# Kernel tuning notes

Measured on AMD Instinct MI355X. Metric: run time of the kernel, lower is better.

The kernel has to match this reference:

```python
import jax, jax.numpy as jnp
import numpy as np

N1, C, T1, V = 16, 64, 512, 25
NH, DK, DV, BD = 8, 64, 64, 64
DKH, DVH = DK // NH, DV // NH
NB = T1 // BD


def rel_to_abs(x):
    # x: (..., L, 2L-1) -> (..., L, L)  (rel-shift trick)
    *lead, L, _ = x.shape
    x = jnp.pad(x, [(0, 0)] * (x.ndim - 1) + [(0, 1)])      # (..., L, 2L)
    x = x.reshape(*lead, L * 2 * L)
    x = jnp.pad(x, [(0, 0)] * (x.ndim - 1) + [(0, L - 1)])
    x = x.reshape(*lead, L + 1, 2 * L - 1)
    return x[..., :L, L - 1:]


def setup_inputs() -> dict:
    key = jax.random.key(0)
    ks = jax.random.split(key, 6)
    return {
        "x": jax.random.normal(ks[0], (N1, C, T1, V), jnp.float32),
        "w_qkv": jax.random.normal(ks[1], (2 * DK + DV, C), jnp.float32) * 0.05,
        "b_qkv": jax.random.normal(ks[2], (2 * DK + DV,), jnp.float32) * 0.01,
        "w_out": jax.random.normal(ks[3], (DV, DV), jnp.float32) * 0.05,
        "b_out": jax.random.normal(ks[4], (DV,), jnp.float32) * 0.01,
        "key_rel": jax.random.normal(ks[5], (2 * BD - 1, DKH), jnp.float32),
    }


def reference(x, w_qkv, b_qkv, w_out, b_out, key_rel):
    B = N1 * V
    # (N1,C,T1,V) -> (N1*V, C, T1); 1x1 qkv conv == GEMM over channels
    xr = x.transpose(0, 3, 1, 2).reshape(B, C, T1)
    qkv = jnp.einsum('oc,bct->bot', w_qkv, xr) + b_qkv[None, :, None]
    q, k, v = qkv[:, :DK], qkv[:, DK:2 * DK], qkv[:, 2 * DK:]
    # split heads and blocks: (B, NH, dh, NB, BD); all blocks vectorized
    q = q.reshape(B, NH, DKH, NB, BD) * (DKH ** -0.5)
    k = k.reshape(B, NH, DKH, NB, BD)
    v = v.reshape(B, NH, DVH, NB, BD)
    logits = jnp.einsum('bhdnt,bhdns->bhnts', q, k)          # (B,NH,NB,BD,BD)
    # relative position logits (rel-shift)
    qb = q.transpose(0, 1, 3, 4, 2)                          # (B,NH,NB,BD,DKH)
    rel = jnp.einsum('bhntd,md->bhntm', qb, key_rel)         # (B,NH,NB,BD,2BD-1)
    logits = logits + rel_to_abs(rel)
    weights = jax.nn.softmax(logits, axis=-1)
    out = jnp.einsum('bhnts,bhdns->bhdnt', weights, v)       # (B,NH,DVH,NB,BD)
    # combine heads (head-major channels) and blocks along T
    out = out.reshape(B, DV, T1)
    ao = jnp.einsum('oc,bct->bot', w_out, out) + b_out[None, :, None]
    ao = ao.reshape(N1, V, DV, T1).transpose(0, 2, 3, 1)     # (N1,DV,T1,V)
    return jax.nn.relu(ao + x)
```

## Files before the change

### kernel.cpp

```cpp
#include <hip/hip_runtime.h>
#include <math.h>

#define Vc 25
#define QSCALE 0.5100697243f

typedef short bf16x8 __attribute__((ext_vector_type(8), may_alias));
typedef unsigned int u32x2a __attribute__((ext_vector_type(2), may_alias));
typedef float f32x4 __attribute__((ext_vector_type(4)));

#define FENCE() asm volatile("" ::: "memory")

__device__ __forceinline__ unsigned short f2bf(float f) {
    unsigned u = __builtin_bit_cast(unsigned, f);
    u = (u + 0x7fff + ((u >> 16) & 1)) >> 16;
    return (unsigned short)u;
}
__device__ __forceinline__ unsigned short f2bf_fast(float f) {
    unsigned u = __builtin_bit_cast(unsigned, f) + 0x8000u;
    return (unsigned short)(u >> 16);
}
__device__ __forceinline__ unsigned pkbf(float lo, float hi) {
    unsigned a = __builtin_bit_cast(unsigned, lo) + 0x8000u;
    unsigned b = __builtin_bit_cast(unsigned, hi) + 0x8000u;
    return __builtin_amdgcn_perm(b, a, 0x07060302);
}
__device__ __forceinline__ float bf2f(unsigned short h) {
    unsigned u = ((unsigned)h) << 16;
    return __builtin_bit_cast(float, u);
}

template<int CTRL>
__device__ __forceinline__ float dpp_add(float x) {
    int xi = __builtin_bit_cast(int, x);
    int yi = __builtin_amdgcn_update_dpp(0, xi, CTRL, 0xf, 0xf, true);
    return x + __builtin_bit_cast(float, yi);
}
__device__ __forceinline__ float row_sum16(float s) {
    s = dpp_add<0xB1>(s);
    s = dpp_add<0x4E>(s);
    s = dpp_add<0x141>(s);
    s = dpp_add<0x140>(s);
    return s;
}

#define WQA_O 0
#define BQ_O  12288
#define KRT_O 12672
#define WOA_O 13760

__global__ void prep_kernel(const float* __restrict__ w_qkv, const float* __restrict__ b_qkv,
                            const float* __restrict__ w_out, const float* __restrict__ key_rel,
                            unsigned short* __restrict__ ws)
{
    const int gid = blockIdx.x * 256 + threadIdx.x;
    const int gsz = gridDim.x * 256;
    for (int id = gid; id < 12288; id += gsz) {
        int j = id & 7, lane = (id >> 3) & 63, ks = (id >> 9) & 1, mt = id >> 10;
        int m = mt * 16 + (lane & 15);
        int k = ks * 32 + (lane >> 4) * 8 + j;
        ws[WQA_O + id] = f2bf(w_qkv[m * 64 + k] * (m < 64 ? QSCALE : 1.f));
    }
    float* bq = (float*)(ws + BQ_O);
    for (int id = gid; id < 192; id += gsz)
        bq[id] = b_qkv[id] * (id < 64 ? QSCALE : 1.f);
    for (int id = gid; id < 1088; id += gsz) {
        int d = id & 7, m = id >> 3;
        ws[KRT_O + id] = (m < 127) ? f2bf(key_rel[m * 8 + d]) : (unsigned short)0;
    }
    for (int id = gid; id < 4096; id += gsz) {
        int j = id & 7, lane = (id >> 3) & 63, mtg = id >> 9;
        int m = (mtg & 3) * 16 + (lane & 15);
        int k = (mtg >> 2) * 32 + (lane >> 4) * 8 + j;
        ws[WOA_O + id] = f2bf(w_out[m * 64 + k]);
    }
}

#define QT_O   0
#define KT_O   4096
#define VS_O   8192
#define OT_O   12800
#define SCR_O  15360
#define SMEM_U16 19968

__global__ __launch_bounds__(256, 4)
void tcn_attn(const float* __restrict__ x, const float* __restrict__ b_out,
              const unsigned short* __restrict__ ws, float* __restrict__ y)
{
    __shared__ unsigned short sm[SMEM_U16];

    const int tid  = threadIdx.x;
    const int lane = tid & 63;
    const int w    = tid >> 6;
    const int li   = lane & 15;
    const int lq   = lane >> 4;
    const int koff = lq * 8;
    const int n    = blockIdx.x;
    const int b    = blockIdx.y;
    const int n1   = b / Vc;
    const int v    = b - n1 * Vc;
    const int t0   = n * 64;
    const int trow = 16 * w + li;
    const unsigned scr = SCR_O + w * 1152;

    const bf16x8 z8 = {0,0,0,0,0,0,0,0};
    const f32x4  z4 = {0.f,0.f,0.f,0.f};

    for (int i = tid; i < 1920; i += 256)
        *(bf16x8*)(sm + i * 8) = z8;

    float xres[16];
    f32x4 pacc[4];
    #pragma unroll
    for (int mt = 0; mt < 4; ++mt)
        #pragma unroll
        for (int r = 0; r < 4; ++r) {
            int o = mt * 16 + lq * 4 + r;
            xres[mt * 4 + r] = x[((n1 * 64 + o) * 512 + t0 + 16 * w + li) * Vc + v];
            pacc[mt][r] = b_out[o];
        }

    #pragma unroll
    for (int mt = 0; mt < 4; ++mt)
        #pragma unroll
        for (int r = 0; r < 4; ++r)
            sm[SCR_O + (16 * w + li) * 72 + mt * 16 + 4 * lq + r] = f2bf_fast(xres[mt * 4 + r]);
    __syncthreads();

    const unsigned short* wq = ws + WQA_O;
    const float* bq = (const float*)(ws + BQ_O);
    #pragma unroll
    for (int sec = 0; sec < 3; ++sec) {
        const int mt = sec * 4 + w;
        bf16x8 a0 = *(const bf16x8*)(wq + ((mt * 2 + 0) * 64 + lane) * 8);
        bf16x8 a1 = *(const bf16x8*)(wq + ((mt * 2 + 1) * 64 + lane) * 8);
        f32x4 acc[4];
        #pragma unroll
        for (int nt = 0; nt < 4; ++nt) {
            #pragma unroll
            for (int r = 0; r < 4; ++r) acc[nt][r] = bq[mt * 16 + lq * 4 + r];
            bf16x8 b0 = *(const bf16x8*)(sm + SCR_O + (16 * nt + li) * 72 + koff);
            bf16x8 b1 = *(const bf16x8*)(sm + SCR_O + (16 * nt + li) * 72 + 32 + koff);
            acc[nt] = __builtin_amdgcn_mfma_f32_16x16x32_bf16(a0, b0, acc[nt], 0, 0, 0);
            acc[nt] = __builtin_amdgcn_mfma_f32_16x16x32_bf16(a1, b1, acc[nt], 0, 0, 0);
        }
        const int h2 = 2 * w + (lq >> 1);
        if (sec < 2) {
            const unsigned base = (sec == 0 ? QT_O : KT_O) + h2 * 512 + (lq & 1) * 4;
            #pragma unroll
            for (int nt = 0; nt < 4; ++nt) {
                u32x2a p;
                p.x = pkbf(acc[nt][0], acc[nt][1]);
                p.y = pkbf(acc[nt][2], acc[nt][3]);
                *(u32x2a*)(sm + base + (16 * nt + li) * 8) = p;
            }
        } else {
            #pragma unroll
            for (int nt = 0; nt < 4; ++nt)
                #pragma unroll
                for (int r = 0; r < 4; ++r)
                    sm[VS_O + h2 * 576 + ((lq & 1) * 4 + r) * 72 + 16 * nt + li] = f2bf_fast(acc[nt][r]);
        }
    }
    __syncthreads();

    bf16x8 br[5];
    #pragma unroll
    for (int j = 0; j < 5; ++j)
        br[j] = *(const bf16x8*)(ws + KRT_O + (16 * (3 - w + j) + li) * 8 + koff);

    int bidx[4];
    bool ghi[4];
    #pragma unroll
    for (int r = 0; r < 4; ++r) {
        int d = li - 4 * lq - r + 15;
        bidx[r] = ((lane & 48) | (d & 15)) << 2;
        ghi[r]  = d >= 16;
    }

    auto FRONT = [&](int h, f32x4* qk, f32x4* rl) {
        bf16x8 aq = *(const bf16x8*)(sm + QT_O + h * 512 + trow * 8 + koff);
        if (lane >= 16) aq = z8;
        #pragma unroll
        for (int nt = 0; nt < 4; ++nt) {
            bf16x8 bk = *(const bf16x8*)(sm + KT_O + h * 512 + (16 * nt + li) * 8 + koff);
            qk[nt] = __builtin_amdgcn_mfma_f32_16x16x32_bf16(aq, bk, z4, 0, 0, 0);
        }
        #pragma unroll
        for (int j = 0; j < 5; ++j)
            rl[j] = __builtin_amdgcn_mfma_f32_16x16x32_bf16(aq, br[j], z4, 0, 0, 0);
    };

    f32x4 qk[4], rl[5];
    FRONT(0, qk, rl);

    #pragma unroll
    for (int h = 0; h < 8; ++h) {
        f32x4 qkn[4], rln[5];
        if (h < 7) FRONT(h + 1, qkn, rln);
        bf16x8 ao[4];
        if ((h & 3) == 3) {
            const int g = h >> 2;
            #pragma unroll
            for (int mt = 0; mt < 4; ++mt)
                ao[mt] = *(const bf16x8*)(ws + WOA_O + ((g * 4 + mt) * 64 + lane) * 8);
        }
        float ex[4][4], lsum[4] = {0.f, 0.f, 0.f, 0.f};
        #pragma unroll
        for (int r = 0; r < 4; ++r) {
            float sr[5];
            #pragma unroll
            for (int j = 0; j < 5; ++j)
                sr[j] = __builtin_bit_cast(float,
                        __builtin_amdgcn_ds_bpermute(bidx[r], __builtin_bit_cast(int, rl[j][r])));
            #pragma unroll
            for (int nt = 0; nt < 4; ++nt) {
                float rv = ghi[r] ? sr[nt + 1] : sr[nt];
                float e = __builtin_amdgcn_exp2f(qk[nt][r] + rv);
                ex[nt][r] = e;
                lsum[r] += e;
            }
        }
        float linv[4];
        #pragma unroll
        for (int r = 0; r < 4; ++r)
            linv[r] = 1.0f / row_sum16(lsum[r]);
        #pragma unroll
        for (int nt = 0; nt < 4; ++nt)
            #pragma unroll
            for (int r = 0; r < 4; ++r)
                sm[scr + (4 * lq + r) * 72 + 16 * nt + li] = f2bf_fast(ex[nt][r]);
        FENCE();
        f32x4 av = z4;
        #pragma unroll
        for (int ks = 0; ks < 2; ++ks) {
            bf16x8 aa = *(const bf16x8*)(sm + scr + li * 72 + ks * 32 + koff);
            bf16x8 bv = *(const bf16x8*)(sm + VS_O + h * 576 + (li & 7) * 72 + ks * 32 + koff);
            av = __builtin_amdgcn_mfma_f32_16x16x32_bf16(aa, bv, av, 0, 0, 0);
        }
        if (li < 8) {
            #pragma unroll
            for (int r = 0; r < 4; ++r)
                sm[OT_O + (16 * w + 4 * lq + r) * 40 + (h & 3) * 8 + li] = f2bf_fast(av[r] * linv[r]);
        }
        if ((h & 3) == 3) {
            FENCE();
            bf16x8 bo = *(const bf16x8*)(sm + OT_O + trow * 40 + koff);
            #pragma unroll
            for (int mt = 0; mt < 4; ++mt)
                pacc[mt] = __builtin_amdgcn_mfma_f32_16x16x32_bf16(ao[mt], bo, pacc[mt], 0, 0, 0);
        }
        FENCE();
        if (h < 7) {
            #pragma unroll
            for (int i = 0; i < 4; ++i) qk[i] = qkn[i];
            #pragma unroll
            for (int j = 0; j < 5; ++j) rl[j] = rln[j];
        }
    }

    #pragma unroll
    for (int mt = 0; mt < 4; ++mt)
        #pragma unroll
        for (int r = 0; r < 4; ++r) {
            int o = mt * 16 + lq * 4 + r;
            int idx = ((n1 * 64 + o) * 512 + t0 + 16 * w + li) * Vc + v;
            y[idx] = fmaxf(pacc[mt][r] + xres[mt * 4 + r], 0.f);
        }
}

extern "C" void kernel_launch(void* const* d_in, const int* in_sizes, int n_in,
                              void* d_out, int out_size, void* d_ws, size_t ws_size,
                              hipStream_t stream) {
    const float* x       = (const float*)d_in[0];
    const float* w_qkv   = (const float*)d_in[1];
    const float* b_qkv   = (const float*)d_in[2];
    const float* w_out   = (const float*)d_in[3];
    const float* b_out   = (const float*)d_in[4];
    const float* key_rel = (const float*)d_in[5];
    float* y = (float*)d_out;
    unsigned short* ws = (unsigned short*)d_ws;

    prep_kernel<<<dim3(96), dim3(256), 0, stream>>>(w_qkv, b_qkv, w_out, key_rel, ws);
    dim3 grid(512 / 64, 400);
    tcn_attn<<<grid, dim3(256), 0, stream>>>(x, b_out, ws, y);
}
```

Measured before the change: 218.1 us.

## Split heads across two wave groups with 512-thread blocks

```diff
diff --git a/kernel.cpp b/kernel.cpp
--- a/kernel.cpp
+++ b/kernel.cpp
@@ -79,10 +79,10 @@
 #define KT_O   4096
 #define VS_O   8192
 #define OT_O   12800
-#define SCR_O  15360
-#define SMEM_U16 19968
-
-__global__ __launch_bounds__(256, 4)
+#define SCR_O  17408
+#define SMEM_U16 26624
+
+__global__ __launch_bounds__(512, 6)
 void tcn_attn(const float* __restrict__ x, const float* __restrict__ b_out,
               const unsigned short* __restrict__ ws, float* __restrict__ y)
 {
@@ -91,6 +91,8 @@
     const int tid  = threadIdx.x;
     const int lane = tid & 63;
     const int w    = tid >> 6;
+    const int rg   = w >> 1;
+    const int hg   = w & 1;
     const int li   = lane & 15;
     const int lq   = lane >> 4;
     const int koff = lq * 8;
@@ -99,66 +101,61 @@
     const int n1   = b / Vc;
     const int v    = b - n1 * Vc;
     const int t0   = n * 64;
-    const int trow = 16 * w + li;
+    const int trow = 16 * rg + li;
     const unsigned scr = SCR_O + w * 1152;
 
     const bf16x8 z8 = {0,0,0,0,0,0,0,0};
     const f32x4  z4 = {0.f,0.f,0.f,0.f};
 
-    for (int i = tid; i < 1920; i += 256)
+    for (int i = tid; i < 2176; i += 512)
         *(bf16x8*)(sm + i * 8) = z8;
 
-    float xres[16];
-    f32x4 pacc[4];
-    #pragma unroll
-    for (int mt = 0; mt < 4; ++mt)
+    float xres[8];
+    f32x4 pacc[2];
+    #pragma unroll
+    for (int mtl = 0; mtl < 2; ++mtl)
         #pragma unroll
         for (int r = 0; r < 4; ++r) {
-            int o = mt * 16 + lq * 4 + r;
-            xres[mt * 4 + r] = x[((n1 * 64 + o) * 512 + t0 + 16 * w + li) * Vc + v];
-            pacc[mt][r] = b_out[o];
-        }
-
-    #pragma unroll
-    for (int mt = 0; mt < 4; ++mt)
+            int o = hg * 32 + mtl * 16 + lq * 4 + r;
+            xres[mtl * 4 + r] = x[((n1 * 64 + o) * 512 + t0 + trow) * Vc + v];
+            pacc[mtl][r] = b_out[o];
+        }
+
+    #pragma unroll
+    for (int mtl = 0; mtl < 2; ++mtl)
         #pragma unroll
         for (int r = 0; r < 4; ++r)
-            sm[SCR_O + (16 * w + li) * 72 + mt * 16 + 4 * lq + r] = f2bf_fast(xres[mt * 4 + r]);
+            sm[SCR_O + trow * 72 + hg * 32 + mtl * 16 + 4 * lq + r] = f2bf_fast(xres[mtl * 4 + r]);
     __syncthreads();
 
     const unsigned short* wq = ws + WQA_O;
     const float* bq = (const float*)(ws + BQ_O);
     #pragma unroll
-    for (int sec = 0; sec < 3; ++sec) {
-        const int mt = sec * 4 + w;
+    for (int i = 0; i < 6; ++i) {
+        const int p  = 6 * w + i;
+        const int mt = p >> 2;
+        const int nt = p & 3;
         bf16x8 a0 = *(const bf16x8*)(wq + ((mt * 2 + 0) * 64 + lane) * 8);
         bf16x8 a1 = *(const bf16x8*)(wq + ((mt * 2 + 1) * 64 + lane) * 8);
-        f32x4 acc[4];
-        #pragma unroll
-        for (int nt = 0; nt < 4; ++nt) {
-            #pragma unroll
-            for (int r = 0; r < 4; ++r) acc[nt][r] = bq[mt * 16 + lq * 4 + r];
-            bf16x8 b0 = *(const bf16x8*)(sm + SCR_O + (16 * nt + li) * 72 + koff);
-            bf16x8 b1 = *(const bf16x8*)(sm + SCR_O + (16 * nt + li) * 72 + 32 + koff);
-            acc[nt] = __builtin_amdgcn_mfma_f32_16x16x32_bf16(a0, b0, acc[nt], 0, 0, 0);
-            acc[nt] = __builtin_amdgcn_mfma_f32_16x16x32_bf16(a1, b1, acc[nt], 0, 0, 0);
-        }
-        const int h2 = 2 * w + (lq >> 1);
-        if (sec < 2) {
-            const unsigned base = (sec == 0 ? QT_O : KT_O) + h2 * 512 + (lq & 1) * 4;
-            #pragma unroll
-            for (int nt = 0; nt < 4; ++nt) {
-                u32x2a p;
-                p.x = pkbf(acc[nt][0], acc[nt][1]);
-                p.y = pkbf(acc[nt][2], acc[nt][3]);
-                *(u32x2a*)(sm + base + (16 * nt + li) * 8) = p;
-            }
+        f32x4 acc;
+        #pragma unroll
+        for (int r = 0; r < 4; ++r) acc[r] = bq[mt * 16 + lq * 4 + r];
+        bf16x8 b0 = *(const bf16x8*)(sm + SCR_O + (16 * nt + li) * 72 + koff);
+        bf16x8 b1 = *(const bf16x8*)(sm + SCR_O + (16 * nt + li) * 72 + 32 + koff);
+        acc = __builtin_amdgcn_mfma_f32_16x16x32_bf16(a0, b0, acc, 0, 0, 0);
+        acc = __builtin_amdgcn_mfma_f32_16x16x32_bf16(a1, b1, acc, 0, 0, 0);
+        const int mt4 = mt & 3;
+        const int h2  = 2 * mt4 + (lq >> 1);
+        if (mt < 8) {
+            const unsigned base = (mt < 4 ? QT_O : KT_O) + h2 * 512 + (lq & 1) * 4;
+            u32x2a pk;
+            pk.x = pkbf(acc[0], acc[1]);
+            pk.y = pkbf(acc[2], acc[3]);
+            *(u32x2a*)(sm + base + (16 * nt + li) * 8) = pk;
         } else {
             #pragma unroll
-            for (int nt = 0; nt < 4; ++nt)
-                #pragma unroll
-                for (int r = 0; r < 4; ++r)
-                    sm[VS_O + h2 * 576 + ((lq & 1) * 4 + r) * 72 + 16 * nt + li] = f2bf_fast(acc[nt][r]);
+            for (int r = 0; r < 4; ++r)
+                sm[VS_O + h2 * 576 + ((lq & 1) * 4 + r) * 72 + 16 * nt + li] = f2bf_fast(acc[r]);
         }
     }
     __syncthreads();
@@ -166,7 +163,7 @@
     bf16x8 br[5];
     #pragma unroll
     for (int j = 0; j < 5; ++j)
-        br[j] = *(const bf16x8*)(ws + KRT_O + (16 * (3 - w + j) + li) * 8 + koff);
+        br[j] = *(const bf16x8*)(ws + KRT_O + (16 * (3 - rg + j) + li) * 8 + koff);
 
     int bidx[4];
     bool ghi[4];
@@ -191,19 +188,13 @@
     };
 
     f32x4 qk[4], rl[5];
-    FRONT(0, qk, rl);
-
-    #pragma unroll
-    for (int h = 0; h < 8; ++h) {
+    FRONT(hg * 4, qk, rl);
+
+    #pragma unroll
+    for (int hh = 0; hh < 4; ++hh) {
+        const int h = hg * 4 + hh;
         f32x4 qkn[4], rln[5];
-        if (h < 7) FRONT(h + 1, qkn, rln);
-        bf16x8 ao[4];
-        if ((h & 3) == 3) {
-            const int g = h >> 2;
-            #pragma unroll
-            for (int mt = 0; mt < 4; ++mt)
-                ao[mt] = *(const bf16x8*)(ws + WOA_O + ((g * 4 + mt) * 64 + lane) * 8);
-        }
+        if (hh < 3) FRONT(h + 1, qkn, rln);
         float ex[4][4], lsum[4] = {0.f, 0.f, 0.f, 0.f};
         #pragma unroll
         for (int r = 0; r < 4; ++r) {
@@ -240,17 +231,10 @@
         if (li < 8) {
             #pragma unroll
             for (int r = 0; r < 4; ++r)
-                sm[OT_O + (16 * w + 4 * lq + r) * 40 + (h & 3) * 8 + li] = f2bf_fast(av[r] * linv[r]);
-        }
-        if ((h & 3) == 3) {
-            FENCE();
-            bf16x8 bo = *(const bf16x8*)(sm + OT_O + trow * 40 + koff);
-            #pragma unroll
-            for (int mt = 0; mt < 4; ++mt)
-                pacc[mt] = __builtin_amdgcn_mfma_f32_16x16x32_bf16(ao[mt], bo, pacc[mt], 0, 0, 0);
+                sm[OT_O + (16 * rg + 4 * lq + r) * 72 + h * 8 + li] = f2bf_fast(av[r] * linv[r]);
         }
         FENCE();
-        if (h < 7) {
+        if (hh < 3) {
             #pragma unroll
             for (int i = 0; i < 4; ++i) qk[i] = qkn[i];
             #pragma unroll
@@ -258,13 +242,25 @@
         }
     }
 
-    #pragma unroll
-    for (int mt = 0; mt < 4; ++mt)
+    __syncthreads();
+    bf16x8 bo0 = *(const bf16x8*)(sm + OT_O + trow * 72 + koff);
+    bf16x8 bo1 = *(const bf16x8*)(sm + OT_O + trow * 72 + 32 + koff);
+    #pragma unroll
+    for (int mtl = 0; mtl < 2; ++mtl) {
+        const int gmt = hg * 2 + mtl;
+        bf16x8 a0 = *(const bf16x8*)(ws + WOA_O + ((0 + gmt) * 64 + lane) * 8);
+        bf16x8 a1 = *(const bf16x8*)(ws + WOA_O + ((4 + gmt) * 64 + lane) * 8);
+        pacc[mtl] = __builtin_amdgcn_mfma_f32_16x16x32_bf16(a0, bo0, pacc[mtl], 0, 0, 0);
+        pacc[mtl] = __builtin_amdgcn_mfma_f32_16x16x32_bf16(a1, bo1, pacc[mtl], 0, 0, 0);
+    }
+
+    #pragma unroll
+    for (int mtl = 0; mtl < 2; ++mtl)
         #pragma unroll
         for (int r = 0; r < 4; ++r) {
-            int o = mt * 16 + lq * 4 + r;
-            int idx = ((n1 * 64 + o) * 512 + t0 + 16 * w + li) * Vc + v;
-            y[idx] = fmaxf(pacc[mt][r] + xres[mt * 4 + r], 0.f);
+            int o = hg * 32 + mtl * 16 + lq * 4 + r;
+            int idx = ((n1 * 64 + o) * 512 + t0 + trow) * Vc + v;
+            y[idx] = fmaxf(pacc[mtl][r] + xres[mtl * 4 + r], 0.f);
         }
 }
 
@@ -282,5 +278,5 @@
 
     prep_kernel<<<dim3(96), dim3(256), 0, stream>>>(w_qkv, b_qkv, w_out, key_rel, ws);
     dim3 grid(512 / 64, 400);
-    tcn_attn<<<grid, dim3(256), 0, stream>>>(x, b_out, ws, y);
-}
+    tcn_attn<<<grid, dim3(512), 0, stream>>>(x, b_out, ws, y);
+}
```

Result: slower. 376.6 us (+72.6%).

## Convert attention kernel to persistent blocks pulling work items from an atomic queue

Applied to the files above, without the earlier changes.

```diff
diff --git a/kernel.cpp b/kernel.cpp
--- a/kernel.cpp
+++ b/kernel.cpp
@@ -3,6 +3,7 @@
 
 #define Vc 25
 #define QSCALE 0.5100697243f
+#define NITEMS 3200
 
 typedef short bf16x8 __attribute__((ext_vector_type(8), may_alias));
 typedef unsigned int u32x2a __attribute__((ext_vector_type(2), may_alias));
@@ -47,6 +48,7 @@
 #define BQ_O  12288
 #define KRT_O 12672
 #define WOA_O 13760
+#define CNT_O 17856
 
 __global__ void prep_kernel(const float* __restrict__ w_qkv, const float* __restrict__ b_qkv,
                             const float* __restrict__ w_out, const float* __restrict__ key_rel,
@@ -54,6 +56,7 @@
 {
     const int gid = blockIdx.x * 256 + threadIdx.x;
     const int gsz = gridDim.x * 256;
+    if (gid == 0) *(unsigned*)(ws + CNT_O) = 0u;
     for (int id = gid; id < 12288; id += gsz) {
         int j = id & 7, lane = (id >> 3) & 63, ks = (id >> 9) & 1, mt = id >> 10;
         int m = mt * 16 + (lane & 15);
@@ -84,9 +87,11 @@
 
 __global__ __launch_bounds__(256, 4)
 void tcn_attn(const float* __restrict__ x, const float* __restrict__ b_out,
-              const unsigned short* __restrict__ ws, float* __restrict__ y)
+              const unsigned short* __restrict__ ws, unsigned* __restrict__ cnt,
+              float* __restrict__ y)
 {
     __shared__ unsigned short sm[SMEM_U16];
+    __shared__ unsigned s_item;
 
     const int tid  = threadIdx.x;
     const int lane = tid & 63;
@@ -94,11 +99,6 @@
     const int li   = lane & 15;
     const int lq   = lane >> 4;
     const int koff = lq * 8;
-    const int n    = blockIdx.x;
-    const int b    = blockIdx.y;
-    const int n1   = b / Vc;
-    const int v    = b - n1 * Vc;
-    const int t0   = n * 64;
     const int trow = 16 * w + li;
     const unsigned scr = SCR_O + w * 1152;
 
@@ -108,60 +108,12 @@
     for (int i = tid; i < 1920; i += 256)
         *(bf16x8*)(sm + i * 8) = z8;
 
-    float xres[16];
-    f32x4 pacc[4];
+    float bias_r[16];
     #pragma unroll
     for (int mt = 0; mt < 4; ++mt)
         #pragma unroll
-        for (int r = 0; r < 4; ++r) {
-            int o = mt * 16 + lq * 4 + r;
-            xres[mt * 4 + r] = x[((n1 * 64 + o) * 512 + t0 + 16 * w + li) * Vc + v];
-            pacc[mt][r] = b_out[o];
-        }
-
-    #pragma unroll
-    for (int mt = 0; mt < 4; ++mt)
-        #pragma unroll
         for (int r = 0; r < 4; ++r)
-            sm[SCR_O + (16 * w + li) * 72 + mt * 16 + 4 * lq + r] = f2bf_fast(xres[mt * 4 + r]);
-    __syncthreads();
-
-    const unsigned short* wq = ws + WQA_O;
-    const float* bq = (const float*)(ws + BQ_O);
-    #pragma unroll
-    for (int sec = 0; sec < 3; ++sec) {
-        const int mt = sec * 4 + w;
-        bf16x8 a0 = *(const bf16x8*)(wq + ((mt * 2 + 0) * 64 + lane) * 8);
-        bf16x8 a1 = *(const bf16x8*)(wq + ((mt * 2 + 1) * 64 + lane) * 8);
-        f32x4 acc[4];
-        #pragma unroll
-        for (int nt = 0; nt < 4; ++nt) {
-            #pragma unroll
-            for (int r = 0; r < 4; ++r) acc[nt][r] = bq[mt * 16 + lq * 4 + r];
-            bf16x8 b0 = *(const bf16x8*)(sm + SCR_O + (16 * nt + li) * 72 + koff);
-            bf16x8 b1 = *(const bf16x8*)(sm + SCR_O + (16 * nt + li) * 72 + 32 + koff);
-            acc[nt] = __builtin_amdgcn_mfma_f32_16x16x32_bf16(a0, b0, acc[nt], 0, 0, 0);
-            acc[nt] = __builtin_amdgcn_mfma_f32_16x16x32_bf16(a1, b1, acc[nt], 0, 0, 0);
-        }
-        const int h2 = 2 * w + (lq >> 1);
-        if (sec < 2) {
-            const unsigned base = (sec == 0 ? QT_O : KT_O) + h2 * 512 + (lq & 1) * 4;
-            #pragma unroll
-            for (int nt = 0; nt < 4; ++nt) {
-                u32x2a p;
-                p.x = pkbf(acc[nt][0], acc[nt][1]);
-                p.y = pkbf(acc[nt][2], acc[nt][3]);
-                *(u32x2a*)(sm + base + (16 * nt + li) * 8) = p;
-            }
-        } else {
-            #pragma unroll
-            for (int nt = 0; nt < 4; ++nt)
-                #pragma unroll
-                for (int r = 0; r < 4; ++r)
-                    sm[VS_O + h2 * 576 + ((lq & 1) * 4 + r) * 72 + 16 * nt + li] = f2bf_fast(acc[nt][r]);
-        }
-    }
-    __syncthreads();
+            bias_r[mt * 4 + r] = b_out[mt * 16 + lq * 4 + r];
 
     bf16x8 br[5];
     #pragma unroll
@@ -190,82 +142,151 @@
             rl[j] = __builtin_amdgcn_mfma_f32_16x16x32_bf16(aq, br[j], z4, 0, 0, 0);
     };
 
-    f32x4 qk[4], rl[5];
-    FRONT(0, qk, rl);
-
-    #pragma unroll
-    for (int h = 0; h < 8; ++h) {
-        f32x4 qkn[4], rln[5];
-        if (h < 7) FRONT(h + 1, qkn, rln);
-        bf16x8 ao[4];
-        if ((h & 3) == 3) {
-            const int g = h >> 2;
-            #pragma unroll
-            for (int mt = 0; mt < 4; ++mt)
-                ao[mt] = *(const bf16x8*)(ws + WOA_O + ((g * 4 + mt) * 64 + lane) * 8);
+    const unsigned short* wq = ws + WQA_O;
+    const float* bq = (const float*)(ws + BQ_O);
+
+    for (;;) {
+        if (tid == 0) s_item = atomicAdd(cnt, 1u);
+        __syncthreads();
+        const unsigned item = s_item;
+        if (item >= NITEMS) break;
+
+        const int n  = item / 400;
+        const int bb = item - n * 400;
+        const int n1 = bb / 25;
+        const int v  = bb - n1 * 25;
+        const int t0 = n * 64;
+
+        float xres[16];
+        f32x4 pacc[4];
+        #pragma unroll
+        for (int mt = 0; mt < 4; ++mt)
+            #pragma unroll
+            for (int r = 0; r < 4; ++r) {
+                int o = mt * 16 + lq * 4 + r;
+                xres[mt * 4 + r] = x[((n1 * 64 + o) * 512 + t0 + 16 * w + li) * Vc + v];
+                pacc[mt][r] = bias_r[mt * 4 + r];
+            }
+
+        #pragma unroll
+        for (int mt = 0; mt < 4; ++mt)
+            #pragma unroll
+            for (int r = 0; r < 4; ++r)
+                sm[SCR_O + (16 * w + li) * 72 + mt * 16 + 4 * lq + r] = f2bf_fast(xres[mt * 4 + r]);
+        __syncthreads();
+
+        #pragma unroll
+        for (int sec = 0; sec < 3; ++sec) {
+            const int mt = sec * 4 + w;
+            bf16x8 a0 = *(const bf16x8*)(wq + ((mt * 2 + 0) * 64 + lane) * 8);
+            bf16x8 a1 = *(const bf16x8*)(wq + ((mt * 2 + 1) * 64 + lane) * 8);
+            f32x4 acc[4];
+            #pragma unroll
+            for (int nt = 0; nt < 4; ++nt) {
+                #pragma unroll
+                for (int r = 0; r < 4; ++r) acc[nt][r] = bq[mt * 16 + lq * 4 + r];
+                bf16x8 b0 = *(const bf16x8*)(sm + SCR_O + (16 * nt + li) * 72 + koff);
+                bf16x8 b1 = *(const bf16x8*)(sm + SCR_O + (16 * nt + li) * 72 + 32 + koff);
+                acc[nt] = __builtin_amdgcn_mfma_f32_16x16x32_bf16(a0, b0, acc[nt], 0, 0, 0);
+                acc[nt] = __builtin_amdgcn_mfma_f32_16x16x32_bf16(a1, b1, acc[nt], 0, 0, 0);
+            }
+            const int h2 = 2 * w + (lq >> 1);
+            if (sec < 2) {
+                const unsigned base = (sec == 0 ? QT_O : KT_O) + h2 * 512 + (lq & 1) * 4;
+                #pragma unroll
+                for (int nt = 0; nt < 4; ++nt) {
+                    u32x2a p;
+                    p.x = pkbf(acc[nt][0], acc[nt][1]);
+                    p.y = pkbf(acc[nt][2], acc[nt][3]);
+                    *(u32x2a*)(sm + base + (16 * nt + li) * 8) = p;
+                }
+            } else {
+                #pragma unroll
+                for (int nt = 0; nt < 4; ++nt)
+                    #pragma unroll
+                    for (int r = 0; r < 4; ++r)
+                        sm[VS_O + h2 * 576 + ((lq & 1) * 4 + r) * 72 + 16 * nt + li] = f2bf_fast(acc[nt][r]);
+            }
         }
-        float ex[4][4], lsum[4] = {0.f, 0.f, 0.f, 0.f};
-        #pragma unroll
-        for (int r = 0; r < 4; ++r) {
-            float sr[5];
-            #pragma unroll
-            for (int j = 0; j < 5; ++j)
-                sr[j] = __builtin_bit_cast(float,
-                        __builtin_amdgcn_ds_bpermute(bidx[r], __builtin_bit_cast(int, rl[j][r])));
-            #pragma unroll
-            for (int nt = 0; nt < 4; ++nt) {
-                float rv = ghi[r] ? sr[nt + 1] : sr[nt];
-                float e = __builtin_amdgcn_exp2f(qk[nt][r] + rv);
-                ex[nt][r] = e;
-                lsum[r] += e;
+        __syncthreads();
+
+        f32x4 qk[4], rl[5];
+        FRONT(0, qk, rl);
+
+        #pragma unroll
+        for (int h = 0; h < 8; ++h) {
+            f32x4 qkn[4], rln[5];
+            if (h < 7) FRONT(h + 1, qkn, rln);
+            bf16x8 ao[4];
+            if ((h & 3) == 3) {
+                const int g = h >> 2;
+                #pragma unroll
+                for (int mt = 0; mt < 4; ++mt)
+                    ao[mt] = *(const bf16x8*)(ws + WOA_O + ((g * 4 + mt) * 64 + lane) * 8);
+            }
+            float ex[4][4], lsum[4] = {0.f, 0.f, 0.f, 0.f};
+            #pragma unroll
+            for (int r = 0; r < 4; ++r) {
+                float sr[5];
+                #pragma unroll
+                for (int j = 0; j < 5; ++j)
+                    sr[j] = __builtin_bit_cast(float,
+                            __builtin_amdgcn_ds_bpermute(bidx[r], __builtin_bit_cast(int, rl[j][r])));
+                #pragma unroll
+                for (int nt = 0; nt < 4; ++nt) {
+                    float rv = ghi[r] ? sr[nt + 1] : sr[nt];
+                    float e = __builtin_amdgcn_exp2f(qk[nt][r] + rv);
+                    ex[nt][r] = e;
+                    lsum[r] += e;
+                }
+            }
+            float linv[4];
+            #pragma unroll
+            for (int r = 0; r < 4; ++r)
+                linv[r] = 1.0f / row_sum16(lsum[r]);
+            #pragma unroll
+            for (int nt = 0; nt < 4; ++nt)
+                #pragma unroll
+                for (int r = 0; r < 4; ++r)
+                    sm[scr + (4 * lq + r) * 72 + 16 * nt + li] = f2bf_fast(ex[nt][r]);
+            FENCE();
+            f32x4 av = z4;
+            #pragma unroll
+            for (int ks = 0; ks < 2; ++ks) {
+                bf16x8 aa = *(const bf16x8*)(sm + scr + li * 72 + ks * 32 + koff);
+                bf16x8 bv = *(const bf16x8*)(sm + VS_O + h * 576 + (li & 7) * 72 + ks * 32 + koff);
+                av = __builtin_amdgcn_mfma_f32_16x16x32_bf16(aa, bv, av, 0, 0, 0);
+            }
+            if (li < 8) {
+                #pragma unroll
+                for (int r = 0; r < 4; ++r)
+                    sm[OT_O + (16 * w + 4 * lq + r) * 40 + (h & 3) * 8 + li] = f2bf_fast(av[r] * linv[r]);
+            }
+            if ((h & 3) == 3) {
+                FENCE();
+                bf16x8 bo = *(const bf16x8*)(sm + OT_O + trow * 40 + koff);
+                #pragma unroll
+                for (int mt = 0; mt < 4; ++mt)
+                    pacc[mt] = __builtin_amdgcn_mfma_f32_16x16x32_bf16(ao[mt], bo, pacc[mt], 0, 0, 0);
+            }
+            FENCE();
+            if (h < 7) {
+                #pragma unroll
+                for (int i = 0; i < 4; ++i) qk[i] = qkn[i];
+                #pragma unroll
+                for (int j = 0; j < 5; ++j) rl[j] = rln[j];
             }
         }
-        float linv[4];
-        #pragma unroll
-        for (int r = 0; r < 4; ++r)
-            linv[r] = 1.0f / row_sum16(lsum[r]);
-        #pragma unroll
-        for (int nt = 0; nt < 4; ++nt)
-            #pragma unroll
-            for (int r = 0; r < 4; ++r)
-                sm[scr + (4 * lq + r) * 72 + 16 * nt + li] = f2bf_fast(ex[nt][r]);
-        FENCE();
-        f32x4 av = z4;
-        #pragma unroll
-        for (int ks = 0; ks < 2; ++ks) {
-            bf16x8 aa = *(const bf16x8*)(sm + scr + li * 72 + ks * 32 + koff);
-            bf16x8 bv = *(const bf16x8*)(sm + VS_O + h * 576 + (li & 7) * 72 + ks * 32 + koff);
-            av = __builtin_amdgcn_mfma_f32_16x16x32_bf16(aa, bv, av, 0, 0, 0);
-        }
-        if (li < 8) {
-            #pragma unroll
-            for (int r = 0; r < 4; ++r)
-                sm[OT_O + (16 * w + 4 * lq + r) * 40 + (h & 3) * 8 + li] = f2bf_fast(av[r] * linv[r]);
-        }
-        if ((h & 3) == 3) {
-            FENCE();
-            bf16x8 bo = *(const bf16x8*)(sm + OT_O + trow * 40 + koff);
-            #pragma unroll
-            for (int mt = 0; mt < 4; ++mt)
-                pacc[mt] = __builtin_amdgcn_mfma_f32_16x16x32_bf16(ao[mt], bo, pacc[mt], 0, 0, 0);
-        }
-        FENCE();
-        if (h < 7) {
-            #pragma unroll
-            for (int i = 0; i < 4; ++i) qk[i] = qkn[i];
-            #pragma unroll
-            for (int j = 0; j < 5; ++j) rl[j] = rln[j];
-        }
-    }
-
-    #pragma unroll
-    for (int mt = 0; mt < 4; ++mt)
-        #pragma unroll
-        for (int r = 0; r < 4; ++r) {
-            int o = mt * 16 + lq * 4 + r;
-            int idx = ((n1 * 64 + o) * 512 + t0 + 16 * w + li) * Vc + v;
-            y[idx] = fmaxf(pacc[mt][r] + xres[mt * 4 + r], 0.f);
-        }
+
+        #pragma unroll
+        for (int mt = 0; mt < 4; ++mt)
+            #pragma unroll
+            for (int r = 0; r < 4; ++r) {
+                int o = mt * 16 + lq * 4 + r;
+                int idx = ((n1 * 64 + o) * 512 + t0 + 16 * w + li) * Vc + v;
+                y[idx] = fmaxf(pacc[mt][r] + xres[mt * 4 + r], 0.f);
+            }
+    }
 }
 
 extern "C" void kernel_launch(void* const* d_in, const int* in_sizes, int n_in,
@@ -279,8 +300,8 @@
     const float* key_rel = (const float*)d_in[5];
     float* y = (float*)d_out;
     unsigned short* ws = (unsigned short*)d_ws;
+    unsigned* cnt = (unsigned*)(ws + CNT_O);
 
     prep_kernel<<<dim3(96), dim3(256), 0, stream>>>(w_qkv, b_qkv, w_out, key_rel, ws);
-    dim3 grid(512 / 64, 400);
-    tcn_attn<<<grid, dim3(256), 0, stream>>>(x, b_out, ws, y);
-}
+    tcn_attn<<<dim3(1024), dim3(256), 0, stream>>>(x, b_out, ws, cnt, y);
+}
```

Measured after the change: 401.4 us. +84.0%, slower.
